# Kernel optimization log

Measured on AMD Instinct MI355X. Metric: run time of the kernel, lower is better.

The kernel has to match this reference:

```python
import jax, jax.numpy as jnp
import numpy as np

B, T_SRC, T_TGT = 1024, 50, 30   # batch, encoder length, decode horizon
I, H = 4, 512                    # input (coord) dim, hidden size; num_layers = 2


def _u(key, shape, scale):
    return jax.random.uniform(key, shape, jnp.float32, -scale, scale)


def setup_inputs() -> dict:
    key = jax.random.key(0)
    ks = jax.random.split(key, 16)
    s = float(1.0 / np.sqrt(H))  # torch LSTM/Linear init range
    return {
        "x": jax.random.normal(ks[0], (B, T_SRC, I), jnp.float32),
        "enc_Wih0": _u(ks[1], (4 * H, I), s), "enc_Whh0": _u(ks[2], (4 * H, H), s), "enc_b0": _u(ks[3], (4 * H,), s),
        "enc_Wih1": _u(ks[4], (4 * H, H), s), "enc_Whh1": _u(ks[5], (4 * H, H), s), "enc_b1": _u(ks[6], (4 * H,), s),
        "dec_Wih0": _u(ks[7], (4 * H, I), s), "dec_Whh0": _u(ks[8], (4 * H, H), s), "dec_b0": _u(ks[9], (4 * H,), s),
        "dec_Wih1": _u(ks[10], (4 * H, H), s), "dec_Whh1": _u(ks[11], (4 * H, H), s), "dec_b1": _u(ks[12], (4 * H,), s),
        "head_W": _u(ks[13], (I, H), s), "head_b": _u(ks[14], (I,), s),
        "target_len": T_TGT,
    }


def _cell(x, h, c, Wih, Whh, b):
    # PyTorch LSTM cell, gate order (i, f, g, o); b = b_ih + b_hh folded.
    gates = x @ Wih.T + h @ Whh.T + b
    i, f, g, o = jnp.split(gates, 4, axis=-1)
    c = jax.nn.sigmoid(f) * c + jax.nn.sigmoid(i) * jnp.tanh(g)
    h = jax.nn.sigmoid(o) * jnp.tanh(c)
    return h, c


def reference(x, enc_Wih0, enc_Whh0, enc_b0, enc_Wih1, enc_Whh1, enc_b1,
              dec_Wih0, dec_Whh0, dec_b0, dec_Wih1, dec_Whh1, dec_b1,
              head_W, head_b, target_len):
    bsz = x.shape[0]
    z = jnp.zeros((bsz, H), x.dtype)

    # ---- encoder: 2-layer LSTM scanned over source time ----
    def enc_step(carry, xt):
        h0, c0, h1, c1 = carry
        h0, c0 = _cell(xt, h0, c0, enc_Wih0, enc_Whh0, enc_b0)
        h1, c1 = _cell(h0, h1, c1, enc_Wih1, enc_Whh1, enc_b1)
        return (h0, c0, h1, c1), None

    (h0, c0, h1, c1), _ = jax.lax.scan(enc_step, (z, z, z, z), jnp.swapaxes(x, 0, 1))

    def dec_step(carry, _):
        inp, h0, c0, h1, c1 = carry
        h0, c0 = _cell(inp, h0, c0, dec_Wih0, dec_Whh0, dec_b0)
        h1, c1 = _cell(h0, h1, c1, dec_Wih1, dec_Whh1, dec_b1)
        out = h1 @ head_W.T + head_b  # [B, I]
        return (out, h0, c0, h1, c1), out

    init = (x[:, -1, :], h0, c0, h1, c1)
    _, outs = jax.lax.scan(dec_step, init, None, length=target_len)
    return jnp.swapaxes(outs, 0, 1)  # [B, target_len, I]
```

## Files before the change

kernel.cpp:

```cpp
#include <hip/hip_runtime.h>
#include <math.h>
#include <stdint.h>

#define B 1024
#define H 512
#define T_SRC 50
#define T_TGT 30
#define I_DIM 4
#define NTHR 256

typedef _Float16 half8 __attribute__((ext_vector_type(8)));
typedef float f32x4 __attribute__((ext_vector_type(4)));
typedef unsigned long long u64;

#define GLOBAL_AS __attribute__((address_space(1)))
#define LDS_AS    __attribute__((address_space(3)))

#define SCALE_F 1099511627776.0f
#define INV_SCALE 8.6736173798840355e-19

__device__ __forceinline__ float sigm(float x) { return 1.0f / (1.0f + expf(-x)); }

__device__ __forceinline__ void layer_core(
    char* smem,
    const _Float16* __restrict__ A1, const _Float16* __restrict__ W1,
    const _Float16* __restrict__ A2, const _Float16* __restrict__ W2,
    int npass, int zero_c,
    const float* __restrict__ xg, int xstride,
    const float* __restrict__ xl,
    const float* __restrict__ Wih,
    const float* __restrict__ bias,
    float* __restrict__ c_st, _Float16* __restrict__ h_out,
    _Float16* pH,
    int m0, int kc0)
{
    const int tid = threadIdx.x;
    const int w = tid >> 6, l = tid & 63;
    const int mw = (w & 1) * 32, nw = (w >> 1) * 32;

    f32x4 acc[2][2] = {};
    const int nt = npass * 8;

    size_t aoff[2], boff[2];
    int ldsw[2];
#pragma unroll
    for (int q = 0; q < 2; ++q) {
        int rowq = (w * 2 + q) * 8 + (l >> 3);
        int gsrc = (l & 7) ^ (rowq & 7);
        aoff[q] = (size_t)(m0 + rowq) * H + gsrc * 8;
        int jg = (rowq >> 4) * H + kc0 + (rowq & 15);
        boff[q] = (size_t)jg * H + gsrc * 8;
        ldsw[q] = (w * 2 + q) * 1024;
    }

    auto stage = [&](int t, int cur) {
        const _Float16* Ap = (t < 8) ? A1 : A2;
        const _Float16* Wp = (t < 8) ? W1 : W2;
        const int koff = (t & 7) * 64;
        char* dbase = smem + cur * 16384;
#pragma unroll
        for (int q = 0; q < 2; ++q) {
            __builtin_amdgcn_global_load_lds(
                (const GLOBAL_AS uint32_t*)(Ap + aoff[q] + koff),
                (LDS_AS uint32_t*)(dbase + ldsw[q]), 16, 0, 0);
            __builtin_amdgcn_global_load_lds(
                (const GLOBAL_AS uint32_t*)(Wp + boff[q] + koff),
                (LDS_AS uint32_t*)(dbase + 8192 + ldsw[q]), 16, 0, 0);
        }
    };

    if (nt > 0) {
        stage(0, 0);
        __syncthreads();
        int cur = 0;
        for (int t = 0; t < nt; ++t) {
            if (t + 1 < nt) stage(t + 1, cur ^ 1);
            const char* ab = smem + cur * 16384;
            const char* bb = ab + 8192;
#pragma unroll
            for (int ks = 0; ks < 2; ++ks) {
                half8 af[2], bf[2];
#pragma unroll
                for (int f = 0; f < 2; ++f) {
                    const int gg = ks * 4 + (l >> 4);
                    const int m = mw + f * 16 + (l & 15);
                    af[f] = *reinterpret_cast<const half8*>(ab + m * 128 + ((gg ^ (m & 7)) * 16));
                    const int n = nw + f * 16 + (l & 15);
                    bf[f] = *reinterpret_cast<const half8*>(bb + n * 128 + ((gg ^ (n & 7)) * 16));
                }
#pragma unroll
                for (int fm = 0; fm < 2; ++fm)
#pragma unroll
                    for (int fn = 0; fn < 2; ++fn)
                        acc[fm][fn] = __builtin_amdgcn_mfma_f32_16x16x32_f16(
                            af[fm], bf[fn], acc[fm][fn], 0, 0, 0);
            }
            __syncthreads();
            cur ^= 1;
        }
    }

    float* Gs = reinterpret_cast<float*>(smem);
#pragma unroll
    for (int fm = 0; fm < 2; ++fm)
#pragma unroll
        for (int fn = 0; fn < 2; ++fn)
#pragma unroll
            for (int r = 0; r < 4; ++r)
                Gs[(mw + fm * 16 + (l >> 4) * 4 + r) * 65 + nw + fn * 16 + (l & 15)] =
                    acc[fm][fn][r];
    __syncthreads();

    {
        const int em = tid & 63;
        const int ekq = tid >> 6;
        const int brow = m0 + em;
        const int kbase = kc0 + ekq * 4;
        float g4[4][4];
#pragma unroll
        for (int gate = 0; gate < 4; ++gate)
#pragma unroll
            for (int j = 0; j < 4; ++j)
                g4[gate][j] = Gs[em * 65 + gate * 16 + ekq * 4 + j]
                            + bias[gate * H + kbase + j];
        if (Wih != nullptr) {
            float x0, x1, x2, x3;
            if (xl != nullptr) {
                x0 = xl[em * 4 + 0]; x1 = xl[em * 4 + 1];
                x2 = xl[em * 4 + 2]; x3 = xl[em * 4 + 3];
            } else {
                const float* xr = xg + (size_t)brow * xstride;
                x0 = xr[0]; x1 = xr[1]; x2 = xr[2]; x3 = xr[3];
            }
#pragma unroll
            for (int gate = 0; gate < 4; ++gate)
#pragma unroll
                for (int j = 0; j < 4; ++j) {
                    const float* wv = &Wih[(size_t)(gate * H + kbase + j) * 4];
                    g4[gate][j] += x0 * wv[0] + x1 * wv[1] + x2 * wv[2] + x3 * wv[3];
                }
        }
        size_t cidx = (size_t)brow * H + kbase;
        f32x4 cold;
        if (zero_c) { cold[0] = cold[1] = cold[2] = cold[3] = 0.f; }
        else        { cold = *reinterpret_cast<const f32x4*>(&c_st[cidx]); }
        f32x4 cnew;
        _Float16 h4[4];
#pragma unroll
        for (int j = 0; j < 4; ++j) {
            float cn = sigm(g4[1][j]) * cold[j] + sigm(g4[0][j]) * tanhf(g4[2][j]);
            cnew[j] = cn;
            h4[j] = (_Float16)(sigm(g4[3][j]) * tanhf(cn));
        }
        *reinterpret_cast<f32x4*>(&c_st[cidx]) = cnew;
        u64 hbits;
        __builtin_memcpy(&hbits, h4, 8);
        *reinterpret_cast<u64*>(h_out + cidx) = hbits;
        if (pH != nullptr) {
#pragma unroll
            for (int j = 0; j < 4; ++j)
                pH[em * 16 + ekq * 4 + j] = h4[j];
        }
    }
}

__global__ __launch_bounds__(NTHR)
void enc_step(int d, const float* __restrict__ x,
              const float* __restrict__ eWih0, const float* __restrict__ eb0,
              const float* __restrict__ eb1,
              const _Float16* __restrict__ eWhh0, const _Float16* __restrict__ eWih1,
              const _Float16* __restrict__ eWhh1,
              float* __restrict__ c0, float* __restrict__ c1,
              _Float16* h0a, _Float16* h0b, _Float16* h1a, _Float16* h1b)
{
    __shared__ __align__(16) char smem[32768];
    const int bx = blockIdx.x;
    const int role = bx >> 9, sub = bx & 511;
    const int m0 = (sub & 15) * 64, kc0 = (sub >> 4) * 16;
    _Float16* h0[2] = {h0a, h0b};
    _Float16* h1[2] = {h1a, h1b};

    if (role == 0) {
        const int t = d;
        if (t >= T_SRC) return;
        const _Float16* A1 = (t == 0) ? nullptr : h0[(t - 1) & 1];
        layer_core(smem, A1, eWhh0, nullptr, nullptr, (t == 0) ? 0 : 1, (t == 0) ? 1 : 0,
                   x + (size_t)t * I_DIM, T_SRC * I_DIM, nullptr,
                   eWih0, eb0, c0, h0[t & 1], nullptr, m0, kc0);
    } else {
        const int t = d - 1;
        if (t < 0) return;
        if (t == 0)
            layer_core(smem, h0[0], eWih1, nullptr, nullptr, 1, 1,
                       nullptr, 0, nullptr, nullptr, eb1, c1, h1[0], nullptr, m0, kc0);
        else
            layer_core(smem, h0[t & 1], eWih1, h1[(t - 1) & 1], eWhh1, 2, 0,
                       nullptr, 0, nullptr, nullptr, eb1, c1, h1[t & 1], nullptr, m0, kc0);
    }
}

__global__ __launch_bounds__(NTHR)
void dec0_step(int t, const float* __restrict__ x,
               const float* __restrict__ dWih0, const float* __restrict__ db0,
               const float* __restrict__ headb,
               const _Float16* __restrict__ dWhh0,
               float* __restrict__ c0,
               _Float16* h0a, _Float16* h0b,
               u64* __restrict__ accA, u64* __restrict__ accB,
               float* __restrict__ outp)
{
    __shared__ __align__(16) char smem[32768];
    __shared__ float decbuf[64 * 4];
    const int sub = blockIdx.x;
    const int m0 = (sub & 15) * 64, kc0 = (sub >> 4) * 16;
    const int ntile = sub >> 4;
    const int tid = threadIdx.x;
    _Float16* h0[2] = {h0a, h0b};

    u64* accCur = (t & 1) ? accB : accA;
    u64* accPrev = (t & 1) ? accA : accB;

    const int row = tid >> 2, o = tid & 3;
    if (ntile == 0)
        accCur[(size_t)(m0 + row) * I_DIM + o] = 0ull;

    const float* xg = nullptr;
    const float* xl = nullptr;
    if (t == 0) {
        xg = x + (size_t)(T_SRC - 1) * I_DIM;
    } else {
        long long v = (long long)accPrev[(size_t)(m0 + row) * I_DIM + o];
        float val = (float)((double)v * (1.0 / 1099511627776.0)) + headb[o];
        decbuf[tid] = val;
        if (ntile == 0)
            outp[((size_t)(m0 + row) * T_TGT + (t - 1)) * I_DIM + o] = val;
        xl = decbuf;
        __syncthreads();
    }

    const _Float16* A1 = (t == 0) ? h0[1] : h0[(t - 1) & 1];
    layer_core(smem, A1, dWhh0, nullptr, nullptr, 1, 0,
               xg, T_SRC * I_DIM, xl, dWih0, db0, c0, h0[t & 1], nullptr, m0, kc0);
}

__global__ __launch_bounds__(NTHR)
void dec1_step(int t, const float* __restrict__ db1,
               const float* __restrict__ headW,
               const _Float16* __restrict__ dWih1, const _Float16* __restrict__ dWhh1,
               float* __restrict__ c1,
               _Float16* h0a, _Float16* h0b, _Float16* h1a, _Float16* h1b,
               u64* __restrict__ accA, u64* __restrict__ accB)
{
    __shared__ __align__(16) char smem[32768];
    __shared__ _Float16 pH[64 * 16];
    const int sub = blockIdx.x;
    const int m0 = (sub & 15) * 64, kc0 = (sub >> 4) * 16;
    const int tid = threadIdx.x;
    _Float16* h0[2] = {h0a, h0b};
    _Float16* h1[2] = {h1a, h1b};

    const _Float16* h1prev = (t == 0) ? h1[1] : h1[(t - 1) & 1];
    layer_core(smem, h0[t & 1], dWih1, h1prev, dWhh1, 2, 0,
               nullptr, 0, nullptr, nullptr, db1, c1, h1[t & 1], pH, m0, kc0);
    __syncthreads();

    u64* accCur = (t & 1) ? accB : accA;
    const int em = tid >> 2, o = tid & 3;
    float s = 0.f;
#pragma unroll
    for (int j = 0; j < 16; ++j)
        s += (float)pH[em * 16 + j] * headW[(size_t)o * H + kc0 + j];
    long long q = (long long)(s * SCALE_F);
    atomicAdd(accCur + ((size_t)(m0 + em) * I_DIM + o), (u64)q);
}

__global__ __launch_bounds__(NTHR)
void final_out(const u64* __restrict__ accLast, const float* __restrict__ headb,
               float* __restrict__ outp)
{
    int i = blockIdx.x * blockDim.x + threadIdx.x;
    if (i < B * I_DIM) {
        int b = i >> 2, o = i & 3;
        long long v = (long long)accLast[i];
        float val = (float)((double)v * (1.0 / 1099511627776.0)) + headb[o];
        outp[((size_t)b * T_TGT + (T_TGT - 1)) * I_DIM + o] = val;
    }
}

__global__ void convert6(const float* __restrict__ s0, const float* __restrict__ s1,
                         const float* __restrict__ s2, const float* __restrict__ s3,
                         const float* __restrict__ s4, const float* __restrict__ s5,
                         _Float16* __restrict__ dst)
{
    const int WN4 = (1 << 20) / 4;
    int i = blockIdx.x * blockDim.x + threadIdx.x;
    int stride = gridDim.x * blockDim.x;
    for (; i < 6 * WN4; i += stride) {
        int seg = i / WN4;
        int off = i - seg * WN4;
        const float* sp = seg == 0 ? s0 : seg == 1 ? s1 : seg == 2 ? s2
                        : seg == 3 ? s3 : seg == 4 ? s4 : s5;
        float4 v = reinterpret_cast<const float4*>(sp)[off];
        _Float16 h4o[4] = {(_Float16)v.x, (_Float16)v.y, (_Float16)v.z, (_Float16)v.w};
        u64 bits;
        __builtin_memcpy(&bits, h4o, 8);
        reinterpret_cast<u64*>(dst)[i] = bits;
    }
}

extern "C" void kernel_launch(void* const* d_in, const int* in_sizes, int n_in,
                              void* d_out, int out_size, void* d_ws, size_t ws_size,
                              hipStream_t stream)
{
    const float* x        = (const float*)d_in[0];
    const float* enc_Wih0 = (const float*)d_in[1];
    const float* enc_Whh0 = (const float*)d_in[2];
    const float* enc_b0   = (const float*)d_in[3];
    const float* enc_Wih1 = (const float*)d_in[4];
    const float* enc_Whh1 = (const float*)d_in[5];
    const float* enc_b1   = (const float*)d_in[6];
    const float* dec_Wih0 = (const float*)d_in[7];
    const float* dec_Whh0 = (const float*)d_in[8];
    const float* dec_b0   = (const float*)d_in[9];
    const float* dec_Wih1 = (const float*)d_in[10];
    const float* dec_Whh1 = (const float*)d_in[11];
    const float* dec_b1   = (const float*)d_in[12];
    const float* head_W   = (const float*)d_in[13];
    const float* head_b   = (const float*)d_in[14];
    float* out = (float*)d_out;

    const size_t MB = 1u << 20;
    char* ws = (char*)d_ws;
    float*    c0     = (float*)(ws + 0 * MB);
    float*    c1     = (float*)(ws + 2 * MB);
    _Float16* h0a    = (_Float16*)(ws + 4 * MB);
    _Float16* h0b    = (_Float16*)(ws + 5 * MB);
    _Float16* h1a    = (_Float16*)(ws + 6 * MB);
    _Float16* h1b    = (_Float16*)(ws + 7 * MB);
    u64*      accA   = (u64*)(ws + 8 * MB);
    u64*      accB   = (u64*)(ws + 8 * MB + 65536);
    _Float16* wf16   = (_Float16*)(ws + 9 * MB);
    _Float16* eWhh0f = wf16 + 0 * (1 << 20);
    _Float16* eWih1f = wf16 + 1 * (1 << 20);
    _Float16* eWhh1f = wf16 + 2 * (1 << 20);
    _Float16* dWhh0f = wf16 + 3 * (1 << 20);
    _Float16* dWih1f = wf16 + 4 * (1 << 20);
    _Float16* dWhh1f = wf16 + 5 * (1 << 20);

    convert6<<<2048, NTHR, 0, stream>>>(enc_Whh0, enc_Wih1, enc_Whh1,
                                        dec_Whh0, dec_Wih1, dec_Whh1, wf16);

    for (int d = 0; d <= T_SRC; ++d)
        enc_step<<<1024, NTHR, 0, stream>>>(d, x, enc_Wih0, enc_b0, enc_b1,
                                            eWhh0f, eWih1f, eWhh1f,
                                            c0, c1, h0a, h0b, h1a, h1b);

    for (int t = 0; t < T_TGT; ++t) {
        dec0_step<<<512, NTHR, 0, stream>>>(t, x, dec_Wih0, dec_b0, head_b,
                                            dWhh0f, c0, h0a, h0b, accA, accB, out);
        dec1_step<<<512, NTHR, 0, stream>>>(t, dec_b1, head_W, dWih1f, dWhh1f,
                                            c1, h0a, h0b, h1a, h1b, accA, accB);
    }
    final_out<<<(B * I_DIM + NTHR - 1) / NTHR, NTHR, 0, stream>>>(
        (T_TGT - 1) & 1 ? accB : accA, head_b, out);
}
```

Before: 1.703 ms.

## Replace per-step kernel launches with persistent kernel using per-row-group barriers

Adds a persistent kernel of 512 blocks that runs all encoder and decoder steps in one launch. Each group of 32 blocks sharing a batch row tile synchronises through an atomic counter barrier instead of a kernel boundary. Per-step h buffers are kept instead of ping-pong so no cross-group sync is needed. The decoder head is computed redundantly per block with a full dot product, which removes the fixed-point atomic accumulation. This is meant to cut launch overhead and global sync cost. It relies on all 512 blocks being co-resident, needs a large workspace, and falls back to the old path when the workspace is smaller.

```diff
diff --git a/kernel.cpp b/kernel.cpp
--- a/kernel.cpp
+++ b/kernel.cpp
@@ -8,6 +8,7 @@
 #define T_TGT 30
 #define I_DIM 4
 #define NTHR 256
+#define NSTEP (T_SRC + T_TGT)
 
 typedef _Float16 half8 __attribute__((ext_vector_type(8)));
 typedef float f32x4 __attribute__((ext_vector_type(4)));
@@ -17,9 +18,12 @@
 #define LDS_AS    __attribute__((address_space(3)))
 
 #define SCALE_F 1099511627776.0f
-#define INV_SCALE 8.6736173798840355e-19
 
 __device__ __forceinline__ float sigm(float x) { return 1.0f / (1.0f + expf(-x)); }
+
+__device__ __forceinline__ void cohs(u64* p, u64 v) {
+    __hip_atomic_store(p, v, __ATOMIC_RELAXED, __HIP_MEMORY_SCOPE_AGENT);
+}
 
 __device__ __forceinline__ void layer_core(
     char* smem,
@@ -32,7 +36,7 @@
     const float* __restrict__ bias,
     float* __restrict__ c_st, _Float16* __restrict__ h_out,
     _Float16* pH,
-    int m0, int kc0)
+    int m0, int kc0, int coh)
 {
     const int tid = threadIdx.x;
     const int w = tid >> 6, l = tid & 63;
@@ -155,7 +159,8 @@
         *reinterpret_cast<f32x4*>(&c_st[cidx]) = cnew;
         u64 hbits;
         __builtin_memcpy(&hbits, h4, 8);
-        *reinterpret_cast<u64*>(h_out + cidx) = hbits;
+        if (coh) cohs(reinterpret_cast<u64*>(h_out + cidx), hbits);
+        else     *reinterpret_cast<u64*>(h_out + cidx) = hbits;
         if (pH != nullptr) {
 #pragma unroll
             for (int j = 0; j < 4; ++j)
@@ -163,6 +168,116 @@
         }
     }
 }
+
+
+struct PP {
+    const float* x;
+    const float* eWih0; const float* eb0; const float* eb1;
+    const float* dWih0; const float* db0; const float* db1;
+    const float* headW; const float* headb;
+    const _Float16* eWhh0f; const _Float16* eWih1f; const _Float16* eWhh1f;
+    const _Float16* dWhh0f; const _Float16* dWih1f; const _Float16* dWhh1f;
+    float* c0; float* c1;
+    _Float16* h0base;
+    _Float16* h1base;
+    uint32_t* flags;
+    float* outp;
+};
+
+__device__ __forceinline__ void grp_barrier2(uint32_t* cnt, uint32_t target)
+{
+    __syncthreads();
+    if (threadIdx.x == 0) {
+        __hip_atomic_fetch_add(cnt, 1u, __ATOMIC_RELAXED, __HIP_MEMORY_SCOPE_AGENT);
+        while (__hip_atomic_load(cnt, __ATOMIC_RELAXED, __HIP_MEMORY_SCOPE_AGENT) < target)
+            __builtin_amdgcn_s_sleep(2);
+    }
+    __syncthreads();
+    asm volatile("" ::: "memory");
+}
+
+__device__ __forceinline__ void head_phase2(
+    const _Float16* __restrict__ h1, const float* __restrict__ W,
+    const float* __restrict__ hb, float* __restrict__ decb,
+    float* __restrict__ outp, int m0, int t)
+{
+    const int tid = threadIdx.x;
+    const int row = tid >> 2, o = tid & 3;
+    const _Float16* hr = h1 + (size_t)(m0 + row) * H;
+    const float* wr = W + o * H;
+    float s = 0.f;
+#pragma unroll 4
+    for (int k = 0; k < H; k += 8) {
+        half8 hv = *reinterpret_cast<const half8*>(hr + k);
+#pragma unroll
+        for (int j = 0; j < 8; ++j) s += (float)hv[j] * wr[k + j];
+    }
+    s += hb[o];
+    decb[row * 4 + o] = s;
+    if (outp != nullptr)
+        outp[((size_t)(m0 + row) * T_TGT + t) * I_DIM + o] = s;
+}
+
+__global__ __launch_bounds__(NTHR, 2)
+void lstm_persist2(PP P)
+{
+    __shared__ __align__(16) char smem[32768];
+    __shared__ float decbuf[64 * 4];
+
+    const int bx = blockIdx.x;
+    const int sxcd = bx & 7;
+    const int q = bx >> 3;
+    const int lowq = q & 15;
+    const int hi = (q >> 4) & 3;
+    const int g = lowq ^ ((hi >> 1) << 3);
+    const int ntile = sxcd * 4 + hi;
+    const int m0 = g * 64;
+    const int kc0 = ntile * 16;
+
+    uint32_t* cnt = P.flags + g * 64;
+    uint32_t bar = 0;
+
+    auto h0buf = [&](int s) { return P.h0base + ((size_t)s << 19); };
+    auto h1buf = [&](int s) { return P.h1base + ((size_t)s << 19); };
+
+    for (int s = 0; s < NSTEP; ++s) {
+        const bool enc = (s < T_SRC);
+        {
+            const _Float16* A1 = (s == 0) ? nullptr : h0buf(s - 1);
+            const _Float16* W1 = enc ? P.eWhh0f : P.dWhh0f;
+            const float* Wih = enc ? P.eWih0 : P.dWih0;
+            const float* b0  = enc ? P.eb0 : P.db0;
+            const float* xg = nullptr; const float* xl = nullptr;
+            if (enc)              xg = P.x + (size_t)s * I_DIM;
+            else if (s == T_SRC)  xg = P.x + (size_t)(T_SRC - 1) * I_DIM;
+            else                  xl = decbuf;
+            layer_core(smem, A1, W1, nullptr, nullptr, (s == 0) ? 0 : 1, (s == 0) ? 1 : 0,
+                       xg, T_SRC * I_DIM, xl, Wih, b0, P.c0, h0buf(s), nullptr,
+                       m0, kc0, 1);
+        }
+        grp_barrier2(cnt, 32u * (++bar));
+        {
+            const _Float16* Wi1 = enc ? P.eWih1f : P.dWih1f;
+            const _Float16* Wh1 = enc ? P.eWhh1f : P.dWhh1f;
+            const float* b1 = enc ? P.eb1 : P.db1;
+            if (s == 0)
+                layer_core(smem, h0buf(0), Wi1, nullptr, nullptr, 1, 1,
+                           nullptr, 0, nullptr, nullptr, b1, P.c1, h1buf(0), nullptr,
+                           m0, kc0, 1);
+            else
+                layer_core(smem, h0buf(s), Wi1, h1buf(s - 1), Wh1, 2, 0,
+                           nullptr, 0, nullptr, nullptr, b1, P.c1, h1buf(s), nullptr,
+                           m0, kc0, 1);
+        }
+        grp_barrier2(cnt, 32u * (++bar));
+        if (!enc) {
+            head_phase2(h1buf(s), P.headW, P.headb, decbuf,
+                        (ntile == 0) ? P.outp : nullptr, m0, s - T_SRC);
+            __syncthreads();
+        }
+    }
+}
+
 
 __global__ __launch_bounds__(NTHR)
 void enc_step(int d, const float* __restrict__ x,
@@ -186,16 +301,16 @@
         const _Float16* A1 = (t == 0) ? nullptr : h0[(t - 1) & 1];
         layer_core(smem, A1, eWhh0, nullptr, nullptr, (t == 0) ? 0 : 1, (t == 0) ? 1 : 0,
                    x + (size_t)t * I_DIM, T_SRC * I_DIM, nullptr,
-                   eWih0, eb0, c0, h0[t & 1], nullptr, m0, kc0);
+                   eWih0, eb0, c0, h0[t & 1], nullptr, m0, kc0, 0);
     } else {
         const int t = d - 1;
         if (t < 0) return;
         if (t == 0)
             layer_core(smem, h0[0], eWih1, nullptr, nullptr, 1, 1,
-                       nullptr, 0, nullptr, nullptr, eb1, c1, h1[0], nullptr, m0, kc0);
+                       nullptr, 0, nullptr, nullptr, eb1, c1, h1[0], nullptr, m0, kc0, 0);
         else
             layer_core(smem, h0[t & 1], eWih1, h1[(t - 1) & 1], eWhh1, 2, 0,
-                       nullptr, 0, nullptr, nullptr, eb1, c1, h1[t & 1], nullptr, m0, kc0);
+                       nullptr, 0, nullptr, nullptr, eb1, c1, h1[t & 1], nullptr, m0, kc0, 0);
     }
 }
 
@@ -240,7 +355,7 @@
 
     const _Float16* A1 = (t == 0) ? h0[1] : h0[(t - 1) & 1];
     layer_core(smem, A1, dWhh0, nullptr, nullptr, 1, 0,
-               xg, T_SRC * I_DIM, xl, dWih0, db0, c0, h0[t & 1], nullptr, m0, kc0);
+               xg, T_SRC * I_DIM, xl, dWih0, db0, c0, h0[t & 1], nullptr, m0, kc0, 0);
 }
 
 __global__ __launch_bounds__(NTHR)
@@ -261,7 +376,7 @@
 
     const _Float16* h1prev = (t == 0) ? h1[1] : h1[(t - 1) & 1];
     layer_core(smem, h0[t & 1], dWih1, h1prev, dWhh1, 2, 0,
-               nullptr, 0, nullptr, nullptr, db1, c1, h1[t & 1], pH, m0, kc0);
+               nullptr, 0, nullptr, nullptr, db1, c1, h1[t & 1], pH, m0, kc0, 0);
     __syncthreads();
 
     u64* accCur = (t & 1) ? accB : accA;
@@ -270,8 +385,8 @@
 #pragma unroll
     for (int j = 0; j < 16; ++j)
         s += (float)pH[em * 16 + j] * headW[(size_t)o * H + kc0 + j];
-    long long q = (long long)(s * SCALE_F);
-    atomicAdd(accCur + ((size_t)(m0 + em) * I_DIM + o), (u64)q);
+    long long qv = (long long)(s * SCALE_F);
+    atomicAdd(accCur + ((size_t)(m0 + em) * I_DIM + o), (u64)qv);
 }
 
 __global__ __launch_bounds__(NTHR)
@@ -285,6 +400,14 @@
         float val = (float)((double)v * (1.0 / 1099511627776.0)) + headb[o];
         outp[((size_t)b * T_TGT + (T_TGT - 1)) * I_DIM + o] = val;
     }
+}
+
+
+__global__ void zero_kernel(float* __restrict__ ptr, int n)
+{
+    int i = blockIdx.x * blockDim.x + threadIdx.x;
+    int stride = gridDim.x * blockDim.x;
+    for (; i < n; i += stride) ptr[i] = 0.f;
 }
 
 __global__ void convert6(const float* __restrict__ s0, const float* __restrict__ s1,
@@ -331,6 +454,40 @@
 
     const size_t MB = 1u << 20;
     char* ws = (char*)d_ws;
+    const size_t PERSIST_NEED = 177 * MB;
+
+    if (ws_size >= PERSIST_NEED) {
+        float*    c0     = (float*)(ws + 0 * MB);
+        float*    c1     = (float*)(ws + 2 * MB);
+        uint32_t* flags  = (uint32_t*)(ws + 4 * MB);
+        _Float16* wf16   = (_Float16*)(ws + 5 * MB);
+        _Float16* h0base = (_Float16*)(ws + 17 * MB);
+        _Float16* h1base = (_Float16*)(ws + 97 * MB);
+
+        zero_kernel<<<1, 256, 0, stream>>>((float*)flags, 1024);
+        convert6<<<2048, NTHR, 0, stream>>>(enc_Whh0, enc_Wih1, enc_Whh1,
+                                            dec_Whh0, dec_Wih1, dec_Whh1, wf16);
+
+        PP P;
+        P.x = x;
+        P.eWih0 = enc_Wih0; P.eb0 = enc_b0; P.eb1 = enc_b1;
+        P.dWih0 = dec_Wih0; P.db0 = dec_b0; P.db1 = dec_b1;
+        P.headW = head_W; P.headb = head_b;
+        P.eWhh0f = wf16 + 0 * (1 << 20);
+        P.eWih1f = wf16 + 1 * (1 << 20);
+        P.eWhh1f = wf16 + 2 * (1 << 20);
+        P.dWhh0f = wf16 + 3 * (1 << 20);
+        P.dWih1f = wf16 + 4 * (1 << 20);
+        P.dWhh1f = wf16 + 5 * (1 << 20);
+        P.c0 = c0; P.c1 = c1;
+        P.h0base = h0base; P.h1base = h1base;
+        P.flags = flags;
+        P.outp = out;
+
+        lstm_persist2<<<dim3(512), dim3(NTHR), 0, stream>>>(P);
+        return;
+    }
+
     float*    c0     = (float*)(ws + 0 * MB);
     float*    c1     = (float*)(ws + 2 * MB);
     _Float16* h0a    = (_Float16*)(ws + 4 * MB);
@@ -340,6 +497,9 @@
     u64*      accA   = (u64*)(ws + 8 * MB);
     u64*      accB   = (u64*)(ws + 8 * MB + 65536);
     _Float16* wf16   = (_Float16*)(ws + 9 * MB);
+
+    convert6<<<2048, NTHR, 0, stream>>>(enc_Whh0, enc_Wih1, enc_Whh1,
+                                        dec_Whh0, dec_Wih1, dec_Whh1, wf16);
     _Float16* eWhh0f = wf16 + 0 * (1 << 20);
     _Float16* eWih1f = wf16 + 1 * (1 << 20);
     _Float16* eWhh1f = wf16 + 2 * (1 << 20);
@@ -347,9 +507,6 @@
     _Float16* dWih1f = wf16 + 4 * (1 << 20);
     _Float16* dWhh1f = wf16 + 5 * (1 << 20);
 
-    convert6<<<2048, NTHR, 0, stream>>>(enc_Whh0, enc_Wih1, enc_Whh1,
-                                        dec_Whh0, dec_Wih1, dec_Whh1, wf16);
-
     for (int d = 0; d <= T_SRC; ++d)
         enc_step<<<1024, NTHR, 0, stream>>>(d, x, enc_Wih0, enc_b0, enc_b1,
                                             eWhh0f, eWih1f, eWhh1f,
```

Result: slower. 2.934 ms (+72.3%).

## Fold decoder head into layer-0 weights and fuse decoder layers per step

Applied to the files above, without the earlier changes.

The linear head is folded algebraically into the decoder layer-0 input weights (Weq = Wih0·headW, with a precomputed bias), so each step feeds on h1prev directly instead of doing a per-step atomic head reduction. The two decoder layers are fused into one kernel per step, with a grid-group spin barrier over the 32 blocks sharing a batch tile; h0 is written with agent-scope atomic stores so other blocks see it. All h1 states are stored and the head is applied once at the end. This adds a K=512 GEMM to layer 0 and relies on co-residency of the spinning blocks, and the fp16 folded weights change rounding.

```diff
diff --git a/kernel.cpp b/kernel.cpp
--- a/kernel.cpp
+++ b/kernel.cpp
@@ -17,9 +17,12 @@
 #define LDS_AS    __attribute__((address_space(3)))
 
 #define SCALE_F 1099511627776.0f
-#define INV_SCALE 8.6736173798840355e-19
 
 __device__ __forceinline__ float sigm(float x) { return 1.0f / (1.0f + expf(-x)); }
+
+__device__ __forceinline__ void cohs(u64* p, u64 v) {
+    __hip_atomic_store(p, v, __ATOMIC_RELAXED, __HIP_MEMORY_SCOPE_AGENT);
+}
 
 __device__ __forceinline__ void layer_core(
     char* smem,
@@ -32,7 +35,7 @@
     const float* __restrict__ bias,
     float* __restrict__ c_st, _Float16* __restrict__ h_out,
     _Float16* pH,
-    int m0, int kc0)
+    int m0, int kc0, int coh)
 {
     const int tid = threadIdx.x;
     const int w = tid >> 6, l = tid & 63;
@@ -155,13 +158,26 @@
         *reinterpret_cast<f32x4*>(&c_st[cidx]) = cnew;
         u64 hbits;
         __builtin_memcpy(&hbits, h4, 8);
-        *reinterpret_cast<u64*>(h_out + cidx) = hbits;
+        if (coh) cohs(reinterpret_cast<u64*>(h_out + cidx), hbits);
+        else     *reinterpret_cast<u64*>(h_out + cidx) = hbits;
         if (pH != nullptr) {
 #pragma unroll
             for (int j = 0; j < 4; ++j)
                 pH[em * 16 + ekq * 4 + j] = h4[j];
         }
     }
+}
+
+__device__ __forceinline__ void grp_barrier32(uint32_t* cnt)
+{
+    __syncthreads();
+    if (threadIdx.x == 0) {
+        __hip_atomic_fetch_add(cnt, 1u, __ATOMIC_RELAXED, __HIP_MEMORY_SCOPE_AGENT);
+        while (__hip_atomic_load(cnt, __ATOMIC_RELAXED, __HIP_MEMORY_SCOPE_AGENT) < 32u)
+            __builtin_amdgcn_s_sleep(2);
+    }
+    __syncthreads();
+    asm volatile("" ::: "memory");
 }
 
 __global__ __launch_bounds__(NTHR)
@@ -186,17 +202,67 @@
         const _Float16* A1 = (t == 0) ? nullptr : h0[(t - 1) & 1];
         layer_core(smem, A1, eWhh0, nullptr, nullptr, (t == 0) ? 0 : 1, (t == 0) ? 1 : 0,
                    x + (size_t)t * I_DIM, T_SRC * I_DIM, nullptr,
-                   eWih0, eb0, c0, h0[t & 1], nullptr, m0, kc0);
+                   eWih0, eb0, c0, h0[t & 1], nullptr, m0, kc0, 0);
     } else {
         const int t = d - 1;
         if (t < 0) return;
         if (t == 0)
             layer_core(smem, h0[0], eWih1, nullptr, nullptr, 1, 1,
-                       nullptr, 0, nullptr, nullptr, eb1, c1, h1[0], nullptr, m0, kc0);
+                       nullptr, 0, nullptr, nullptr, eb1, c1, h1[0], nullptr, m0, kc0, 0);
         else
             layer_core(smem, h0[t & 1], eWih1, h1[(t - 1) & 1], eWhh1, 2, 0,
-                       nullptr, 0, nullptr, nullptr, eb1, c1, h1[t & 1], nullptr, m0, kc0);
-    }
+                       nullptr, 0, nullptr, nullptr, eb1, c1, h1[t & 1], nullptr, m0, kc0, 0);
+    }
+}
+
+__global__ __launch_bounds__(NTHR)
+void dec_fused(int t, const float* __restrict__ x,
+               const float* __restrict__ dWih0, const float* __restrict__ db0,
+               const float* __restrict__ db0pc, const float* __restrict__ db1,
+               const _Float16* __restrict__ Weqf,
+               const _Float16* __restrict__ dWhh0f,
+               const _Float16* __restrict__ dWih1f, const _Float16* __restrict__ dWhh1f,
+               float* __restrict__ c0, float* __restrict__ c1,
+               const _Float16* __restrict__ h0prev, const _Float16* __restrict__ h1prev,
+               _Float16* __restrict__ h0cur, _Float16* __restrict__ h1cur,
+               uint32_t* __restrict__ cnt)
+{
+    __shared__ __align__(16) char smem[32768];
+    const int sub = blockIdx.x;
+    const int m0 = (sub & 15) * 64, kc0 = (sub >> 4) * 16;
+    const int g = sub & 15;
+
+    if (t == 0)
+        layer_core(smem, h0prev, dWhh0f, nullptr, nullptr, 1, 0,
+                   x + (size_t)(T_SRC - 1) * I_DIM, T_SRC * I_DIM, nullptr,
+                   dWih0, db0, c0, h0cur, nullptr, m0, kc0, 1);
+    else
+        layer_core(smem, h0prev, dWhh0f, h1prev, Weqf, 2, 0,
+                   nullptr, 0, nullptr, nullptr, db0pc, c0, h0cur, nullptr, m0, kc0, 1);
+
+    grp_barrier32(cnt + g);
+
+    layer_core(smem, h0cur, dWih1f, h1prev, dWhh1f, 2, 0,
+               nullptr, 0, nullptr, nullptr, db1, c1, h1cur, nullptr, m0, kc0, 0);
+}
+
+__global__ __launch_bounds__(NTHR)
+void final_head(const _Float16* __restrict__ h1base, const float* __restrict__ W,
+                const float* __restrict__ hb, float* __restrict__ outp)
+{
+    const int t = blockIdx.x, chunk = blockIdx.y;
+    const _Float16* h1 = h1base + ((size_t)t << 19);
+    const int row = chunk * 64 + (threadIdx.x >> 2), o = threadIdx.x & 3;
+    const _Float16* hr = h1 + (size_t)row * H;
+    const float* wr = W + o * H;
+    float s = 0.f;
+#pragma unroll 4
+    for (int k = 0; k < H; k += 8) {
+        half8 hv = *reinterpret_cast<const half8*>(hr + k);
+#pragma unroll
+        for (int j = 0; j < 8; ++j) s += (float)hv[j] * wr[k + j];
+    }
+    outp[((size_t)row * T_TGT + t) * I_DIM + o] = s + hb[o];
 }
 
 __global__ __launch_bounds__(NTHR)
@@ -240,7 +306,7 @@
 
     const _Float16* A1 = (t == 0) ? h0[1] : h0[(t - 1) & 1];
     layer_core(smem, A1, dWhh0, nullptr, nullptr, 1, 0,
-               xg, T_SRC * I_DIM, xl, dWih0, db0, c0, h0[t & 1], nullptr, m0, kc0);
+               xg, T_SRC * I_DIM, xl, dWih0, db0, c0, h0[t & 1], nullptr, m0, kc0, 0);
 }
 
 __global__ __launch_bounds__(NTHR)
@@ -261,7 +327,7 @@
 
     const _Float16* h1prev = (t == 0) ? h1[1] : h1[(t - 1) & 1];
     layer_core(smem, h0[t & 1], dWih1, h1prev, dWhh1, 2, 0,
-               nullptr, 0, nullptr, nullptr, db1, c1, h1[t & 1], pH, m0, kc0);
+               nullptr, 0, nullptr, nullptr, db1, c1, h1[t & 1], pH, m0, kc0, 0);
     __syncthreads();
 
     u64* accCur = (t & 1) ? accB : accA;
@@ -270,8 +336,8 @@
 #pragma unroll
     for (int j = 0; j < 16; ++j)
         s += (float)pH[em * 16 + j] * headW[(size_t)o * H + kc0 + j];
-    long long q = (long long)(s * SCALE_F);
-    atomicAdd(accCur + ((size_t)(m0 + em) * I_DIM + o), (u64)q);
+    long long qv = (long long)(s * SCALE_F);
+    atomicAdd(accCur + ((size_t)(m0 + em) * I_DIM + o), (u64)qv);
 }
 
 __global__ __launch_bounds__(NTHR)
@@ -285,6 +351,13 @@
         float val = (float)((double)v * (1.0 / 1099511627776.0)) + headb[o];
         outp[((size_t)b * T_TGT + (T_TGT - 1)) * I_DIM + o] = val;
     }
+}
+
+__global__ void zero_kernel(float* __restrict__ ptr, int n)
+{
+    int i = blockIdx.x * blockDim.x + threadIdx.x;
+    int stride = gridDim.x * blockDim.x;
+    for (; i < n; i += stride) ptr[i] = 0.f;
 }
 
 __global__ void convert6(const float* __restrict__ s0, const float* __restrict__ s1,
@@ -305,6 +378,26 @@
         u64 bits;
         __builtin_memcpy(&bits, h4o, 8);
         reinterpret_cast<u64*>(dst)[i] = bits;
+    }
+}
+
+__global__ void weq_build(const float* __restrict__ Wih0, const float* __restrict__ headW,
+                          const float* __restrict__ headb, const float* __restrict__ db0,
+                          _Float16* __restrict__ Weqf, float* __restrict__ db0pc)
+{
+    int i = blockIdx.x * blockDim.x + threadIdx.x;
+    int stride = gridDim.x * blockDim.x;
+    for (int idx = i; idx < 2048 * 512; idx += stride) {
+        int j = idx >> 9, k = idx & 511;
+        const float* wr = &Wih0[(size_t)j * 4];
+        float s = wr[0] * headW[0 * H + k] + wr[1] * headW[1 * H + k]
+                + wr[2] * headW[2 * H + k] + wr[3] * headW[3 * H + k];
+        Weqf[idx] = (_Float16)s;
+    }
+    for (int j = i; j < 2048; j += stride) {
+        const float* wr = &Wih0[(size_t)j * 4];
+        db0pc[j] = db0[j] + wr[0] * headb[0] + wr[1] * headb[1]
+                 + wr[2] * headb[2] + wr[3] * headb[3];
     }
 }
 
@@ -331,6 +424,54 @@
 
     const size_t MB = 1u << 20;
     char* ws = (char*)d_ws;
+    const size_t PRIMARY_NEED = 88 * MB;
+
+    if (ws_size >= PRIMARY_NEED) {
+        float*    c0     = (float*)(ws + 0 * MB);
+        float*    c1     = (float*)(ws + 2 * MB);
+        uint32_t* dflags = (uint32_t*)(ws + 4 * MB);
+        _Float16* wf16   = (_Float16*)(ws + 5 * MB);
+        _Float16* Weqf   = (_Float16*)(ws + 17 * MB);
+        float*    db0pc  = (float*)(ws + 19 * MB);
+        _Float16* h0a    = (_Float16*)(ws + 20 * MB);
+        _Float16* h0b    = (_Float16*)(ws + 21 * MB);
+        _Float16* h1a    = (_Float16*)(ws + 22 * MB);
+        _Float16* h1b    = (_Float16*)(ws + 23 * MB);
+        _Float16* h0d    = (_Float16*)(ws + 24 * MB);
+        _Float16* h1d    = (_Float16*)(ws + 54 * MB);
+
+        _Float16* eWhh0f = wf16 + 0 * (1 << 20);
+        _Float16* eWih1f = wf16 + 1 * (1 << 20);
+        _Float16* eWhh1f = wf16 + 2 * (1 << 20);
+        _Float16* dWhh0f = wf16 + 3 * (1 << 20);
+        _Float16* dWih1f = wf16 + 4 * (1 << 20);
+        _Float16* dWhh1f = wf16 + 5 * (1 << 20);
+
+        zero_kernel<<<2, 256, 0, stream>>>((float*)dflags, 30 * 16);
+        convert6<<<2048, NTHR, 0, stream>>>(enc_Whh0, enc_Wih1, enc_Whh1,
+                                            dec_Whh0, dec_Wih1, dec_Whh1, wf16);
+        weq_build<<<2048, NTHR, 0, stream>>>(dec_Wih0, head_W, head_b, dec_b0,
+                                             Weqf, db0pc);
+
+        for (int d = 0; d <= T_SRC; ++d)
+            enc_step<<<1024, NTHR, 0, stream>>>(d, x, enc_Wih0, enc_b0, enc_b1,
+                                                eWhh0f, eWih1f, eWhh1f,
+                                                c0, c1, h0a, h0b, h1a, h1b);
+
+        for (int t = 0; t < T_TGT; ++t) {
+            const _Float16* h0prev = (t == 0) ? h0b : h0d + ((size_t)(t - 1) << 19);
+            const _Float16* h1prev = (t == 0) ? h1b : h1d + ((size_t)(t - 1) << 19);
+            dec_fused<<<512, NTHR, 0, stream>>>(t, x, dec_Wih0, dec_b0, db0pc, dec_b1,
+                                                Weqf, dWhh0f, dWih1f, dWhh1f,
+                                                c0, c1, h0prev, h1prev,
+                                                h0d + ((size_t)t << 19),
+                                                h1d + ((size_t)t << 19),
+                                                dflags + t * 16);
+        }
+        final_head<<<dim3(T_TGT, 16), NTHR, 0, stream>>>(h1d, head_W, head_b, out);
+        return;
+    }
+
     float*    c0     = (float*)(ws + 0 * MB);
     float*    c1     = (float*)(ws + 2 * MB);
     _Float16* h0a    = (_Float16*)(ws + 4 * MB);
@@ -340,6 +481,9 @@
     u64*      accA   = (u64*)(ws + 8 * MB);
     u64*      accB   = (u64*)(ws + 8 * MB + 65536);
     _Float16* wf16   = (_Float16*)(ws + 9 * MB);
+
+    convert6<<<2048, NTHR, 0, stream>>>(enc_Whh0, enc_Wih1, enc_Whh1,
+                                        dec_Whh0, dec_Wih1, dec_Whh1, wf16);
     _Float16* eWhh0f = wf16 + 0 * (1 << 20);
     _Float16* eWih1f = wf16 + 1 * (1 << 20);
     _Float16* eWhh1f = wf16 + 2 * (1 << 20);
@@ -347,9 +491,6 @@
     _Float16* dWih1f = wf16 + 4 * (1 << 20);
     _Float16* dWhh1f = wf16 + 5 * (1 << 20);
 
-    convert6<<<2048, NTHR, 0, stream>>>(enc_Whh0, enc_Wih1, enc_Whh1,
-                                        dec_Whh0, dec_Wih1, dec_Whh1, wf16);
-
     for (int d = 0; d <= T_SRC; ++d)
         enc_step<<<1024, NTHR, 0, stream>>>(d, x, enc_Wih0, enc_b0, enc_b1,
                                             eWhh0f, eWih1f, eWhh1f,
```

Result: slower. 1.869 ms (+9.8%).

## Triple-buffer LDS K-loop with vmcnt waits and XCD-aware block mapping

Applied to the files above, without the earlier changes.

The GEMM K-loop in layer_core moves from a double-buffered pipeline with two full __syncthreads per tile to a three-stage LDS ring. It keeps two async global-to-LDS loads in flight and waits with s_waitcnt vmcnt plus a single s_barrier. Blocks are also remapped so consecutive block IDs (round-robin across the 8 XCDs) share the same weight column tile. This aims to improve L2 reuse of weights per XCD. In exchange, LDS per block grows from 32KB to 48KB, which may lower occupancy, and the hand-written vmcnt counts depend on the exact number of outstanding loads.

```diff
diff --git a/kernel.cpp b/kernel.cpp
--- a/kernel.cpp
+++ b/kernel.cpp
@@ -17,9 +17,18 @@
 #define LDS_AS    __attribute__((address_space(3)))
 
 #define SCALE_F 1099511627776.0f
-#define INV_SCALE 8.6736173798840355e-19
+#define SMEM_BYTES 49152
 
 __device__ __forceinline__ float sigm(float x) { return 1.0f / (1.0f + expf(-x)); }
+
+__device__ __forceinline__ void sub_map(int sub, int& m0, int& kc0, int& ntile)
+{
+    const int xcd = sub & 7, j = sub >> 3;
+    ntile = xcd * 4 + (j >> 4);
+    const int g = j & 15;
+    m0 = g * 64;
+    kc0 = ntile * 16;
+}
 
 __device__ __forceinline__ void layer_core(
     char* smem,
@@ -53,11 +62,11 @@
         ldsw[q] = (w * 2 + q) * 1024;
     }
 
-    auto stage = [&](int t, int cur) {
+    auto issue = [&](int t, int buf) {
         const _Float16* Ap = (t < 8) ? A1 : A2;
         const _Float16* Wp = (t < 8) ? W1 : W2;
         const int koff = (t & 7) * 64;
-        char* dbase = smem + cur * 16384;
+        char* dbase = smem + buf * 16384;
 #pragma unroll
         for (int q = 0; q < 2; ++q) {
             __builtin_amdgcn_global_load_lds(
@@ -70,12 +79,18 @@
     };
 
     if (nt > 0) {
-        stage(0, 0);
-        __syncthreads();
-        int cur = 0;
+        issue(0, 0);
+        issue(1, 1);
+        int cbuf = 0, ibuf = 2;
         for (int t = 0; t < nt; ++t) {
-            if (t + 1 < nt) stage(t + 1, cur ^ 1);
-            const char* ab = smem + cur * 16384;
+            if (t < nt - 1) asm volatile("s_waitcnt vmcnt(4)" ::: "memory");
+            else            asm volatile("s_waitcnt vmcnt(0)" ::: "memory");
+            __builtin_amdgcn_s_barrier();
+            if (t + 2 < nt) {
+                issue(t + 2, ibuf);
+                ibuf = (ibuf == 2) ? 0 : ibuf + 1;
+            }
+            const char* ab = smem + cbuf * 16384;
             const char* bb = ab + 8192;
 #pragma unroll
             for (int ks = 0; ks < 2; ++ks) {
@@ -95,9 +110,9 @@
                         acc[fm][fn] = __builtin_amdgcn_mfma_f32_16x16x32_f16(
                             af[fm], bf[fn], acc[fm][fn], 0, 0, 0);
             }
-            __syncthreads();
-            cur ^= 1;
-        }
+            cbuf = (cbuf == 2) ? 0 : cbuf + 1;
+        }
+        __syncthreads();
     }
 
     float* Gs = reinterpret_cast<float*>(smem);
@@ -173,10 +188,11 @@
               float* __restrict__ c0, float* __restrict__ c1,
               _Float16* h0a, _Float16* h0b, _Float16* h1a, _Float16* h1b)
 {
-    __shared__ __align__(16) char smem[32768];
+    __shared__ __align__(16) char smem[SMEM_BYTES];
     const int bx = blockIdx.x;
     const int role = bx >> 9, sub = bx & 511;
-    const int m0 = (sub & 15) * 64, kc0 = (sub >> 4) * 16;
+    int m0, kc0, ntile;
+    sub_map(sub, m0, kc0, ntile);
     _Float16* h0[2] = {h0a, h0b};
     _Float16* h1[2] = {h1a, h1b};
 
@@ -209,11 +225,11 @@
                u64* __restrict__ accA, u64* __restrict__ accB,
                float* __restrict__ outp)
 {
-    __shared__ __align__(16) char smem[32768];
+    __shared__ __align__(16) char smem[SMEM_BYTES];
     __shared__ float decbuf[64 * 4];
     const int sub = blockIdx.x;
-    const int m0 = (sub & 15) * 64, kc0 = (sub >> 4) * 16;
-    const int ntile = sub >> 4;
+    int m0, kc0, ntile;
+    sub_map(sub, m0, kc0, ntile);
     const int tid = threadIdx.x;
     _Float16* h0[2] = {h0a, h0b};
 
@@ -251,10 +267,11 @@
                _Float16* h0a, _Float16* h0b, _Float16* h1a, _Float16* h1b,
                u64* __restrict__ accA, u64* __restrict__ accB)
 {
-    __shared__ __align__(16) char smem[32768];
+    __shared__ __align__(16) char smem[SMEM_BYTES];
     __shared__ _Float16 pH[64 * 16];
     const int sub = blockIdx.x;
-    const int m0 = (sub & 15) * 64, kc0 = (sub >> 4) * 16;
+    int m0, kc0, ntile;
+    sub_map(sub, m0, kc0, ntile);
     const int tid = threadIdx.x;
     _Float16* h0[2] = {h0a, h0b};
     _Float16* h1[2] = {h1a, h1b};
@@ -270,8 +287,8 @@
 #pragma unroll
     for (int j = 0; j < 16; ++j)
         s += (float)pH[em * 16 + j] * headW[(size_t)o * H + kc0 + j];
-    long long q = (long long)(s * SCALE_F);
-    atomicAdd(accCur + ((size_t)(m0 + em) * I_DIM + o), (u64)q);
+    long long qv = (long long)(s * SCALE_F);
+    atomicAdd(accCur + ((size_t)(m0 + em) * I_DIM + o), (u64)qv);
 }
 
 __global__ __launch_bounds__(NTHR)
@@ -340,6 +357,9 @@
     u64*      accA   = (u64*)(ws + 8 * MB);
     u64*      accB   = (u64*)(ws + 8 * MB + 65536);
     _Float16* wf16   = (_Float16*)(ws + 9 * MB);
+
+    convert6<<<2048, NTHR, 0, stream>>>(enc_Whh0, enc_Wih1, enc_Whh1,
+                                        dec_Whh0, dec_Wih1, dec_Whh1, wf16);
     _Float16* eWhh0f = wf16 + 0 * (1 << 20);
     _Float16* eWih1f = wf16 + 1 * (1 << 20);
     _Float16* eWhh1f = wf16 + 2 * (1 << 20);
@@ -347,9 +367,6 @@
     _Float16* dWih1f = wf16 + 4 * (1 << 20);
     _Float16* dWhh1f = wf16 + 5 * (1 << 20);
 
-    convert6<<<2048, NTHR, 0, stream>>>(enc_Whh0, enc_Wih1, enc_Whh1,
-                                        dec_Whh0, dec_Wih1, dec_Whh1, wf16);
-
     for (int d = 0; d <= T_SRC; ++d)
         enc_step<<<1024, NTHR, 0, stream>>>(d, x, enc_Wih0, enc_b0, enc_b1,
                                             eWhh0f, eWih1f, eWhh1f,
```

New measurement: 1.572 ms (median of 2 runs). 1.08x faster.
